# Performance work log

Hardware: AMD Instinct MI355X
Metric: run time of the kernel (lower is better)

The kernel has to match this reference:

```python
import jax, jax.numpy as jnp
import numpy as np

N0, N1, N2 = 32768, 8192, 2048
DEG = 8
E0, E1, E2 = N0 * DEG, N1 * DEG, N2 * DEG
C = 32
OUT = 40
EPS = 1e-9


def setup_inputs() -> dict:
    key = jax.random.key(0)
    ks = jax.random.split(key, 32)
    w = lambda k, s, sc=0.1: jax.random.normal(k, s, jnp.float32) * sc
    d = {}
    d['pos0'] = jax.random.normal(ks[0], (N0, 3), jnp.float32)
    d['v0'] = jax.random.normal(ks[1], (N0, 1, 3), jnp.float32)
    # attention layer weights: 10 layers total (2 per block x 5 blocks)
    d['Wq_first'] = w(ks[2], (1, C)); d['Wk_first'] = w(ks[3], (1, C))
    d['Wv_first'] = w(ks[4], (1, C)); d['Wskip_first'] = w(ks[5], (1, C))
    d['Wq_mid'] = w(ks[6], (8, C, C)); d['Wk_mid'] = w(ks[7], (8, C, C))
    d['Wv_mid'] = w(ks[8], (8, C, C)); d['Wskip_mid'] = w(ks[9], (8, C, C))
    d['Wq_last'] = w(ks[10], (C, 1)); d['Wk_last'] = w(ks[11], (C, 1))
    d['Wv_last'] = w(ks[12], (C, 1)); d['Wskip_last'] = w(ks[13], (C, 1))
    d['wr1'] = w(ks[14], (10, 1, 16)); d['wr2'] = w(ks[15], (10, 16, 1))
    d['scale_mid'] = jnp.ones((9, C), jnp.float32)
    d['bias_mid'] = jnp.zeros((9, C), jnp.float32)
    d['scale_last'] = jnp.ones((1,), jnp.float32)
    d['bias_last'] = jnp.zeros((1,), jnp.float32)
    d['Wmlp'] = w(ks[16], (3, OUT))
    d['src0'] = jax.random.randint(ks[17], (E0,), 0, N0)
    d['dst0'] = jax.random.randint(ks[18], (E0,), 0, N0)
    d['src1'] = jax.random.randint(ks[19], (E1,), 0, N1)
    d['dst1'] = jax.random.randint(ks[20], (E1,), 0, N1)
    d['src2'] = jax.random.randint(ks[21], (E2,), 0, N2)
    d['dst2'] = jax.random.randint(ks[22], (E2,), 0, N2)
    d['fp_idx1'] = jax.random.permutation(ks[23], N0)[:N1]
    d['fp_idx2'] = jax.random.permutation(ks[24], N1)[:N2]
    d['cluster1'] = jax.random.randint(ks[25], (N0,), 0, N1)
    d['cluster2'] = jax.random.randint(ks[26], (N1,), 0, N2)
    return d


def _attn(x, src, dst, rel, r, Wq, Wk, Wv, Ws, w1, w2, n):
    # x: [n, Cin, 3] type-1 fiber; equivariant linear maps mix channels only
    q = jnp.einsum('ncv,co->nov', x, Wq)
    k = jnp.einsum('ncv,co->nov', x, Wk)
    v = jnp.einsum('ncv,co->nov', x, Wv)
    logits = jnp.einsum('eov,eov->e', q[dst], k[src]) / np.float32(np.sqrt(3.0 * Wq.shape[1]))
    logits = logits + (jax.nn.relu(r @ w1) @ w2)[:, 0]  # radial (invariant) edge bias
    m = jax.ops.segment_max(logits, dst, num_segments=n)
    ex = jnp.exp(logits - m[dst])
    z = jax.ops.segment_sum(ex, dst, num_segments=n)
    alpha = ex / (z[dst] + EPS)
    msg = (v[src] + rel[:, None, :]) * alpha[:, None, None]  # x_ij='add'
    agg = jax.ops.segment_sum(msg, dst, num_segments=n)
    return agg + jnp.einsum('ncv,co->nov', x, Ws)  # learnable skip


def _norm_bias(x, scale, bias):
    # GNormBias: nonlinearity on invariant norm, preserve direction
    nrm = jnp.sqrt(jnp.sum(x * x, axis=-1, keepdims=True) + 1e-12)
    return jax.nn.relu(scale[None, :, None] * nrm + bias[None, :, None]) * (x / nrm)


def _segmean(x, seg, n):
    s = jax.ops.segment_sum(x, seg, num_segments=n)
    c = jax.ops.segment_sum(jnp.ones((seg.shape[0], 1, 1), x.dtype), seg, num_segments=n)
    return s / (c + EPS)


def reference(pos0, v0, Wq_first, Wk_first, Wv_first, Wskip_first, Wq_mid, Wk_mid, Wv_mid, Wskip_mid, Wq_last, Wk_last, Wv_last, Wskip_last, wr1, wr2, scale_mid, bias_mid, scale_last, bias_last, Wmlp, src0, dst0, src1, dst1, src2, dst2, fp_idx1, fp_idx2, cluster1, cluster2):
    def edge_geo(pos, src, dst):
        rel = pos[dst] - pos[src]
        r = jnp.sqrt(jnp.sum(rel * rel, -1, keepdims=True) + 1e-12)
        return rel, r

    rel0, r0 = edge_geo(pos0, src0, dst0)
    pos1 = pos0[fp_idx1]
    rel1, r1 = edge_geo(pos1, src1, dst1)
    pos2 = pos1[fp_idx2]
    rel2, r2 = edge_geo(pos2, src2, dst2)

    def layer(i, x, Wq, Wk, Wv, Ws, sc, bi, src, dst, rel, r, n):
        return _norm_bias(_attn(x, src, dst, rel, r, Wq, Wk, Wv, Ws, wr1[i], wr2[i], n), sc, bi)

    # down block 0 (level 0)
    x = layer(0, v0, Wq_first, Wk_first, Wv_first, Wskip_first, scale_mid[0], bias_mid[0], src0, dst0, rel0, r0, N0)
    x0 = layer(1, x, Wq_mid[0], Wk_mid[0], Wv_mid[0], Wskip_mid[0], scale_mid[1], bias_mid[1], src0, dst0, rel0, r0, N0)
    # FPS pool -> level 1, down block 1
    x = _segmean(x0, cluster1, N1)
    x = layer(2, x, Wq_mid[1], Wk_mid[1], Wv_mid[1], Wskip_mid[1], scale_mid[2], bias_mid[2], src1, dst1, rel1, r1, N1)
    x1 = layer(3, x, Wq_mid[2], Wk_mid[2], Wv_mid[2], Wskip_mid[2], scale_mid[3], bias_mid[3], src1, dst1, rel1, r1, N1)
    # FPS pool -> level 2, bottleneck
    x = _segmean(x1, cluster2, N2)
    x = layer(4, x, Wq_mid[3], Wk_mid[3], Wv_mid[3], Wskip_mid[3], scale_mid[4], bias_mid[4], src2, dst2, rel2, r2, N2)
    x = layer(5, x, Wq_mid[4], Wk_mid[4], Wv_mid[4], Wskip_mid[4], scale_mid[5], bias_mid[5], src2, dst2, rel2, r2, N2)
    # upsample to level 1 via fp_idx scatter + residual skip, up block 0
    x = jnp.zeros((N1, C, 3), x.dtype).at[fp_idx2].set(x) + x1
    x = layer(6, x, Wq_mid[5], Wk_mid[5], Wv_mid[5], Wskip_mid[5], scale_mid[6], bias_mid[6], src1, dst1, rel1, r1, N1)
    x = layer(7, x, Wq_mid[6], Wk_mid[6], Wv_mid[6], Wskip_mid[6], scale_mid[7], bias_mid[7], src1, dst1, rel1, r1, N1)
    # upsample to level 0 + residual skip, up block 1 (out fiber {1:1})
    x = jnp.zeros((N0, C, 3), x.dtype).at[fp_idx1].set(x) + x0
    x = layer(8, x, Wq_mid[7], Wk_mid[7], Wv_mid[7], Wskip_mid[7], scale_mid[8], bias_mid[8], src0, dst0, rel0, r0, N0)
    x = layer(9, x, Wq_last, Wk_last, Wv_last, Wskip_last, scale_last, bias_last, src0, dst0, rel0, r0, N0)
    # MLP head: [N0,1,3] -> (B=1, N0, 3) -> Linear(3, OUT, no bias) + ReLU
    y = jax.nn.relu(jnp.einsum('bnf,fo->bno', x.reshape(1, N0, 3), Wmlp))
    return y
```

## Files before the change

kernel.cpp:

```cpp
#include <hip/hip_runtime.h>
#include <math.h>

#define N0 32768
#define N1 8192
#define N2 2048
#define E0 262144
#define E1 65536
#define E2 16384
#define NTOT (N0+N1+N2)
#define ETOT (E0+E1+E2)
#define NBLK (NTOT/256)
#define EPS 1e-9f

static inline int cdiv(int a, int b){ return (a + b - 1) / b; }

__device__ inline unsigned bfpack(float a, float b){
  unsigned ua = __float_as_uint(a), ub = __float_as_uint(b);
  ua = (ua + 0x7fffu + ((ua >> 16) & 1u)) >> 16;
  ub = (ub + 0x7fffu + ((ub >> 16) & 1u)) & 0xffff0000u;
  return ua | ub;
}
__device__ inline float bf_lo(unsigned d){ return __uint_as_float(d << 16); }
__device__ inline float bf_hi(unsigned d){ return __uint_as_float(d & 0xffff0000u); }

__device__ inline float grp32_sum(float x){
  x += __int_as_float(__builtin_amdgcn_update_dpp(0, __float_as_int(x), 0x121, 0xf, 0xf, true));
  x += __int_as_float(__builtin_amdgcn_update_dpp(0, __float_as_int(x), 0x122, 0xf, 0xf, true));
  x += __int_as_float(__builtin_amdgcn_update_dpp(0, __float_as_int(x), 0x124, 0xf, 0xf, true));
  x += __int_as_float(__builtin_amdgcn_update_dpp(0, __float_as_int(x), 0x128, 0xf, 0xf, true));
  x += __int_as_float(__builtin_amdgcn_ds_swizzle(__float_as_int(x), 0x401F));
  return x;
}

__global__ void k_gather_pos(const float* __restrict__ pos, const int* __restrict__ idx,
                             float* __restrict__ out, int n){
  int i = blockIdx.x*256 + threadIdx.x;
  if (i < n){
    int s = idx[i];
    out[i*3+0] = pos[s*3+0];
    out[i*3+1] = pos[s*3+1];
    out[i*3+2] = pos[s*3+2];
  }
}
__global__ void k_inv_build(const int* __restrict__ fp, int* __restrict__ inv, int n2){
  int i = blockIdx.x*256 + threadIdx.x;
  if (i < n2) inv[fp[i]] = i;
}

__global__ void k_countA(const int* __restrict__ d0, const int* __restrict__ d1,
                         const int* __restrict__ d2, int* cnt){
  int e = blockIdx.x*256 + threadIdx.x;
  if (e < E0)            atomicAdd(&cnt[d0[e]], 1);
  else if (e < E0+E1)    atomicAdd(&cnt[N0 + d1[e-E0]], 1);
  else if (e < ETOT)     atomicAdd(&cnt[N0+N1 + d2[e-E0-E1]], 1);
}
__global__ __launch_bounds__(256) void k_scan1(const int* __restrict__ cnt,
                                               int* __restrict__ excl,
                                               int* __restrict__ bsum){
  __shared__ int lds[256];
  int tid = threadIdx.x;
  int i = blockIdx.x*256 + tid;
  int v = cnt[i];
  lds[tid] = v;
  __syncthreads();
  for (int off = 1; off < 256; off <<= 1){
    int t = (tid >= off) ? lds[tid - off] : 0;
    __syncthreads();
    lds[tid] += t;
    __syncthreads();
  }
  excl[i] = lds[tid] - v;
  if (tid == 255) bsum[blockIdx.x] = lds[255];
}
__global__ __launch_bounds__(256) void k_scan2(int* bsum, int nb){
  __shared__ int lds[256];
  int tid = threadIdx.x;
  int v = (tid < nb) ? bsum[tid] : 0;
  lds[tid] = v;
  __syncthreads();
  for (int off = 1; off < 256; off <<= 1){
    int t = (tid >= off) ? lds[tid - off] : 0;
    __syncthreads();
    lds[tid] += t;
    __syncthreads();
  }
  if (tid < nb) bsum[tid] = lds[tid] - v;
}
__global__ __launch_bounds__(256) void k_scan3(const int* __restrict__ excl,
                                               const int* __restrict__ bsum,
                                               int* __restrict__ row,
                                               int* __restrict__ cur){
  int i = blockIdx.x*256 + threadIdx.x;
  int r = excl[i] + bsum[blockIdx.x];
  row[i] = r; cur[i] = r;
  if (i == 0) row[NTOT] = ETOT;
}
__global__ void k_scatter_geoA(const int* __restrict__ s0, const int* __restrict__ d0,
                               const int* __restrict__ s1, const int* __restrict__ d1,
                               const int* __restrict__ s2, const int* __restrict__ d2,
                               const float* __restrict__ pos0, const float* __restrict__ pos1,
                               const float* __restrict__ pos2, int* cur,
                               int* __restrict__ srcs, float4* __restrict__ meta){
  int e = blockIdx.x*256 + threadIdx.x;
  if (e >= ETOT) return;
  int s, d, noff; const float* pos;
  if (e < E0)        { s = s0[e];        d = d0[e];        pos = pos0; noff = 0; }
  else if (e < E0+E1){ s = s1[e-E0];     d = d1[e-E0];     pos = pos1; noff = N0; }
  else               { s = s2[e-E0-E1];  d = d2[e-E0-E1];  pos = pos2; noff = N0+N1; }
  float dx = pos[d*3+0]-pos[s*3+0];
  float dy = pos[d*3+1]-pos[s*3+1];
  float dz = pos[d*3+2]-pos[s*3+2];
  int p = atomicAdd(&cur[noff + d], 1);
  srcs[p] = s;
  meta[p] = make_float4(sqrtf(dx*dx+dy*dy+dz*dz+1e-12f), dx, dy, dz);
}

__global__ __launch_bounds__(256) void k_rbias(const float4* __restrict__ meta,
                                               const float* __restrict__ w1,
                                               const float* __restrict__ w2,
                                               float* __restrict__ rb, int nE){
  int e = blockIdx.x*256 + threadIdx.x;
  if (e >= nE) return;
  float r = meta[e].x;
  float a = 0.f;
  #pragma unroll
  for (int j = 0; j < 16; ++j) a += fmaxf(r*w1[j], 0.f)*w2[j];
  rb[e] = a;
}

__global__ __launch_bounds__(256) void k_transformF(
    const float* __restrict__ x, const float* __restrict__ cntv,
    const float* __restrict__ up, const int* __restrict__ inv,
    const float* __restrict__ Wq, const float* __restrict__ Wk,
    const float* __restrict__ Wv, const float* __restrict__ Ws,
    float* __restrict__ q, unsigned* __restrict__ kv, float* __restrict__ s,
    int n, int Cin, int mode){
  __shared__ float wI[4096];
  __shared__ float xr4[8][128];
  __shared__ float kvst[8][192];
  int tid = threadIdx.x;
  int nw = Cin * 32;
  for (int i = tid; i < nw; i += 256){
    wI[i*4+0] = Wq[i]; wI[i*4+1] = Wk[i]; wI[i*4+2] = Wv[i]; wI[i*4+3] = Ws[i];
  }
  int g = tid >> 5, lane = tid & 31;
  int node = blockIdx.x*8 + g;
  int xl = Cin * 3;
  if (node < n){
    if (mode == 1){
      float ic = 1.f / (cntv[node] + EPS);
      for (int c = lane; c < Cin; c += 32){
        int b = node*xl + c*3;
        xr4[g][c*4+0] = x[b+0]*ic; xr4[g][c*4+1] = x[b+1]*ic; xr4[g][c*4+2] = x[b+2]*ic;
      }
    } else if (mode == 2){
      int a = inv[node];
      for (int c = lane; c < Cin; c += 32){
        int b = node*xl + c*3;
        float v0_ = x[b], v1_ = x[b+1], v2_ = x[b+2];
        if (a >= 0){
          size_t ub = (size_t)a*xl + c*3;
          v0_ += up[ub]; v1_ += up[ub+1]; v2_ += up[ub+2];
        }
        xr4[g][c*4+0] = v0_; xr4[g][c*4+1] = v1_; xr4[g][c*4+2] = v2_;
      }
    } else {
      for (int c = lane; c < Cin; c += 32){
        int b = node*xl + c*3;
        xr4[g][c*4+0] = x[b]; xr4[g][c*4+1] = x[b+1]; xr4[g][c*4+2] = x[b+2];
      }
    }
  }
  __syncthreads();
  if (node < n){
    float aq0=0.f,aq1=0.f,aq2=0.f, ak0=0.f,ak1=0.f,ak2=0.f;
    float aw0=0.f,aw1=0.f,aw2=0.f, as0=0.f,as1=0.f,as2=0.f;
    for (int c = 0; c < Cin; ++c){
      float4 xv = *(const float4*)&xr4[g][c*4];
      float4 wv = *(const float4*)&wI[(c*32+lane)*4];
      aq0 += xv.x*wv.x; aq1 += xv.y*wv.x; aq2 += xv.z*wv.x;
      ak0 += xv.x*wv.y; ak1 += xv.y*wv.y; ak2 += xv.z*wv.y;
      aw0 += xv.x*wv.z; aw1 += xv.y*wv.z; aw2 += xv.z*wv.z;
      as0 += xv.x*wv.w; as1 += xv.y*wv.w; as2 += xv.z*wv.w;
    }
    int o = node*96 + lane*3;
    q[o]=aq0; q[o+1]=aq1; q[o+2]=aq2;
    s[o]=as0; s[o+1]=as1; s[o+2]=as2;
    kvst[g][lane*3+0]=ak0; kvst[g][lane*3+1]=ak1; kvst[g][lane*3+2]=ak2;
    kvst[g][96+lane*3+0]=aw0; kvst[g][96+lane*3+1]=aw1; kvst[g][96+lane*3+2]=aw2;
    float2 p0 = *(const float2*)&kvst[g][2*lane];
    float2 p1 = *(const float2*)&kvst[g][64+2*lane];
    float2 p2 = *(const float2*)&kvst[g][128+2*lane];
    *(uint2*)(kv + (size_t)node*96 + 2*lane) = make_uint2(bfpack(p0.x,p0.y), bfpack(p1.x,p1.y));
    kv[(size_t)node*96 + 64 + lane] = bfpack(p2.x, p2.y);
  }
}

#define ATTN_CORE(QB,KVB,SB) \
  float rw1 = (lane < 16) ? wr1[lane] : 0.f; \
  float rw2 = (lane < 16) ? wr2[lane] : 0.f; \
  float ql0=0.f, ql1=0.f, ql2=0.f, ql3=0.f; \
  float z=0.f, av0=0.f, av1=0.f, av2=0.f, av3=0.f, R0=0.f, R1=0.f, R2=0.f; \
  int beg=0, end=0; \
  if (act){ \
    int nb = node*96; \
    float2 qa = *(const float2*)(QB + nb + 2*lane); \
    ql0 = qa.x*invsc; ql1 = qa.y*invsc; \
    if (lane < 16){ \
      float2 qc = *(const float2*)(QB + nb + 64 + 2*lane); \
      ql2 = qc.x*invsc; ql3 = qc.y*invsc; \
    } \
    beg = row[node]; end = row[node+1]; \
  } \
  for (int cb = beg; cb < end; cb += 32){ \
    int csz = end - cb; if (csz > 32) csz = 32; \
    int sn_l = 0; float4 mt = make_float4(0.f,0.f,0.f,0.f); \
    if (lane < csz){ \
      int idx = cb + lane; \
      sn_l = srcs[idx]; \
      mt = meta[idx]; \
    } \
    for (int j = 0; j < csz; j += 4){ \
      int gs = csz - j; if (gs > 4) gs = 4; \
      int sid[4]; float rrB[4]; \
      _Pragma("unroll") \
      for (int t = 0; t < 4; ++t){ \
        int sl = (j + t) & 31; \
        sid[t] = __shfl(sn_l, sl, 32); \
        rrB[t] = __shfl(mt.x, sl, 32); \
      } \
      unsigned d0[4], d1[4], d2[4]; \
      _Pragma("unroll") \
      for (int t = 0; t < 4; ++t){ \
        const unsigned* kp = KVB + (size_t)sid[t]*96; \
        bool ok = t < gs; \
        uint2 ab = ok ? *(const uint2*)(kp + 2*lane) : make_uint2(0u,0u); \
        d0[t] = ab.x; d1[t] = ab.y; \
        d2[t] = ok ? kp[64 + lane] : 0u; \
      } \
      _Pragma("unroll") \
      for (int t = 0; t < 4; ++t){ \
        float pt = bf_lo(d0[t])*ql0 + bf_hi(d0[t])*ql1; \
        if (lane < 16) pt += bf_lo(d1[t])*ql2 + bf_hi(d1[t])*ql3; \
        pt += fmaxf(rrB[t]*rw1, 0.f) * rw2; \
        pt = grp32_sum(pt); \
        float w = (t < gs) ? __expf(fminf(pt, 80.f)) : 0.f; \
        z += w; \
        av0 += w*bf_lo(d2[t]); av1 += w*bf_hi(d2[t]); \
        if (lane >= 16){ av2 += w*bf_lo(d1[t]); av3 += w*bf_hi(d1[t]); } \
        if (lane == j + t){ R0 += w*mt.y; R1 += w*mt.z; R2 += w*mt.w; } \
      } \
    } \
  } \
  R0 = grp32_sum(R0); \
  R1 = grp32_sum(R1); \
  R2 = grp32_sum(R2); \
  if (act){ \
    vsum[g][2*lane+32] = av0; \
    vsum[g][2*lane+33] = av1; \
    if (lane >= 16){ vsum[g][2*lane-32] = av2; vsum[g][2*lane-31] = av3; } \
  } \
  float y0=0.f, y1=0.f, y2=0.f; \
  if (act){ \
    float invz = 1.f / (z + EPS); \
    int base = node*96 + 3*lane; \
    y0 = (vsum[g][3*lane+0] + R0)*invz + SB[base]; \
    y1 = (vsum[g][3*lane+1] + R1)*invz + SB[base+1]; \
    y2 = (vsum[g][3*lane+2] + R2)*invz + SB[base+2]; \
    float nrm = sqrtf(y0*y0 + y1*y1 + y2*y2 + 1e-12f); \
    float f = fmaxf(scaleA[lane]*nrm + biasA[lane], 0.f) / nrm; \
    y0 *= f; y1 *= f; y2 *= f; \
  }

__global__ __launch_bounds__(256) void k_attn32(
    const float* __restrict__ qb, const unsigned* __restrict__ kvb,
    const float* __restrict__ sb,
    const int* __restrict__ row, const int* __restrict__ srcs,
    const float4* __restrict__ meta,
    const float* __restrict__ wr1, const float* __restrict__ wr2,
    const float* __restrict__ scaleA, const float* __restrict__ biasA,
    float* __restrict__ outb,
    float* psum, float* pcnt_, const int* __restrict__ cl,
    int n, float invsc){
  __shared__ float vsum[8][96];
  int tid = threadIdx.x, g = tid >> 5, lane = tid & 31;
  int node = blockIdx.x*8 + g;
  bool act = node < n;
  ATTN_CORE(qb, kvb, sb)
  if (act){
    int base = node*96 + 3*lane;
    outb[base]   = y0;
    outb[base+1] = y1;
    outb[base+2] = y2;
    if (cl){
      int c = cl[node];
      atomicAdd(&psum[c*96 + 3*lane],   y0);
      atomicAdd(&psum[c*96 + 3*lane+1], y1);
      atomicAdd(&psum[c*96 + 3*lane+2], y2);
      if (lane == 0) atomicAdd(&pcnt_[c], 1.f);
    }
  }
}

__global__ __launch_bounds__(256) void k_attn32_t32(
    float* __restrict__ qb, const unsigned* __restrict__ kvin,
    float* __restrict__ sb,
    const int* __restrict__ row, const int* __restrict__ srcs,
    const float4* __restrict__ meta,
    const float* __restrict__ wr1, const float* __restrict__ wr2,
    const float* __restrict__ scaleA, const float* __restrict__ biasA,
    const float* __restrict__ Wq2, const float* __restrict__ Wk2,
    const float* __restrict__ Wv2, const float* __restrict__ Ws2,
    unsigned* __restrict__ kvout, int n, float invsc){
  __shared__ float vsum[8][96];
  __shared__ float wI[4096];
  __shared__ float kvst[8][192];
  int tid = threadIdx.x, g = tid >> 5, lane = tid & 31;
  for (int i = tid; i < 1024; i += 256){
    wI[i*4+0] = Wq2[i]; wI[i*4+1] = Wk2[i]; wI[i*4+2] = Wv2[i]; wI[i*4+3] = Ws2[i];
  }
  int node = blockIdx.x*8 + g;
  bool act = node < n;
  ATTN_CORE(qb, kvin, sb)
  __syncthreads();
  if (act){
    vsum[g][3*lane+0] = y0;
    vsum[g][3*lane+1] = y1;
    vsum[g][3*lane+2] = y2;
    float aq0=0.f,aq1=0.f,aq2=0.f, ak0=0.f,ak1=0.f,ak2=0.f;
    float aw0=0.f,aw1=0.f,aw2=0.f, as0=0.f,as1=0.f,as2=0.f;
    for (int c = 0; c < 32; ++c){
      float x0 = vsum[g][c*3+0], x1 = vsum[g][c*3+1], x2 = vsum[g][c*3+2];
      float4 wv = *(const float4*)&wI[(c*32+lane)*4];
      aq0 += x0*wv.x;  aq1 += x1*wv.x;  aq2 += x2*wv.x;
      ak0 += x0*wv.y;  ak1 += x1*wv.y;  ak2 += x2*wv.y;
      aw0 += x0*wv.z;  aw1 += x1*wv.z;  aw2 += x2*wv.z;
      as0 += x0*wv.w;  as1 += x1*wv.w;  as2 += x2*wv.w;
    }
    int ob = node*96 + 3*lane;
    qb[ob]=aq0; qb[ob+1]=aq1; qb[ob+2]=aq2;
    sb[ob]=as0; sb[ob+1]=as1; sb[ob+2]=as2;
    kvst[g][lane*3+0]=ak0; kvst[g][lane*3+1]=ak1; kvst[g][lane*3+2]=ak2;
    kvst[g][96+lane*3+0]=aw0; kvst[g][96+lane*3+1]=aw1; kvst[g][96+lane*3+2]=aw2;
    float2 p0 = *(const float2*)&kvst[g][2*lane];
    float2 p1 = *(const float2*)&kvst[g][64+2*lane];
    float2 p2 = *(const float2*)&kvst[g][128+2*lane];
    *(uint2*)(kvout + (size_t)node*96 + 2*lane) = make_uint2(bfpack(p0.x,p0.y), bfpack(p1.x,p1.y));
    kvout[(size_t)node*96 + 64 + lane] = bfpack(p2.x, p2.y);
  }
}

__global__ __launch_bounds__(256) void k_attn32_t1(
    const float* __restrict__ qb, const unsigned* __restrict__ kvin,
    const float* __restrict__ sb,
    const int* __restrict__ row, const int* __restrict__ srcs,
    const float4* __restrict__ meta,
    const float* __restrict__ wr1, const float* __restrict__ wr2,
    const float* __restrict__ scaleA, const float* __restrict__ biasA,
    const float* __restrict__ Wq2, const float* __restrict__ Wk2,
    const float* __restrict__ Wv2, const float* __restrict__ Ws2,
    float* __restrict__ q1, float* __restrict__ kv1,
    float* __restrict__ s1,
    int n, float invsc){
  __shared__ float vsum[8][96];
  int tid = threadIdx.x, g = tid >> 5, lane = tid & 31;
  int node = blockIdx.x*8 + g;
  bool act = node < n;
  ATTN_CORE(qb, kvin, sb)
  if (act){
    vsum[g][3*lane+0] = y0;
    vsum[g][3*lane+1] = y1;
    vsum[g][3*lane+2] = y2;
  }
  if (act && lane < 12){
    int m = lane / 3, v = lane - m*3;
    const float* W = (m==0) ? Wq2 : (m==1) ? Wk2 : (m==2) ? Wv2 : Ws2;
    float a = 0.f;
    for (int c = 0; c < 32; ++c) a += vsum[g][c*3+v] * W[c];
    if (m==0)      q1[node*3 + v] = a;
    else if (m==1) kv1[(size_t)node*8 + v] = a;
    else if (m==2) kv1[(size_t)node*8 + 3 + v] = a;
    else           s1[node*3 + v] = a;
  }
}

__global__ __launch_bounds__(256) void k_attn1_head(
    const float* __restrict__ qb, const float* __restrict__ kv1,
    const float* __restrict__ sb, const float* __restrict__ rb9,
    const int* __restrict__ row, const int* __restrict__ srcs,
    const float4* __restrict__ meta,
    const float* __restrict__ scaleA, const float* __restrict__ biasA,
    const float* __restrict__ Wmlp,
    float* __restrict__ out, int n, float invsc){
  __shared__ float w[120];
  int tid = threadIdx.x;
  if (tid < 120) w[tid] = Wmlp[tid];
  __syncthreads();
  int i = blockIdx.x*32 + (tid >> 3);
  int lane8 = tid & 7;
  if (i >= n) return;
  float q0 = qb[i*3]*invsc, q1 = qb[i*3+1]*invsc, q2 = qb[i*3+2]*invsc;
  float z = 0.f, a0 = 0.f, a1 = 0.f, a2 = 0.f;
  int beg = row[i], end = row[i+1];
  for (int e = beg + lane8; e < end; e += 8){
    int s = srcs[e];
    float4 m = meta[e];
    float4 A = *(const float4*)(kv1 + (size_t)s*8);
    float2 B = *(const float2*)(kv1 + (size_t)s*8 + 4);
    float pt = q0*A.x + q1*A.y + q2*A.z + rb9[e];
    float wgt = __expf(fminf(pt, 80.f));
    z += wgt;
    a0 += wgt*(A.w + m.y); a1 += wgt*(B.x + m.z); a2 += wgt*(B.y + m.w);
  }
  #pragma unroll
  for (int xm = 1; xm <= 4; xm <<= 1){
    z  += __shfl_xor(z,  xm, 8);
    a0 += __shfl_xor(a0, xm, 8);
    a1 += __shfl_xor(a1, xm, 8);
    a2 += __shfl_xor(a2, xm, 8);
  }
  float invz = 1.f / (z + EPS);
  float y0 = a0*invz + sb[i*3];
  float y1 = a1*invz + sb[i*3+1];
  float y2 = a2*invz + sb[i*3+2];
  float nrm = sqrtf(y0*y0 + y1*y1 + y2*y2 + 1e-12f);
  float f = fmaxf(scaleA[0]*nrm + biasA[0], 0.f) / nrm;
  y0 *= f; y1 *= f; y2 *= f;
  #pragma unroll
  for (int c = 0; c < 5; ++c){
    int o2 = lane8*5 + c;
    out[(size_t)i*40 + o2] = fmaxf(y0*w[o2] + y1*w[40+o2] + y2*w[80+o2], 0.f);
  }
}

extern "C" void kernel_launch(void* const* d_in, const int* in_sizes, int n_in,
                              void* d_out, int out_size, void* d_ws, size_t ws_size,
                              hipStream_t stream){
  const float* pos0      = (const float*)d_in[0];
  const float* v0        = (const float*)d_in[1];
  const float* Wq_first  = (const float*)d_in[2];
  const float* Wk_first  = (const float*)d_in[3];
  const float* Wv_first  = (const float*)d_in[4];
  const float* Ws_first  = (const float*)d_in[5];
  const float* Wq_mid    = (const float*)d_in[6];
  const float* Wk_mid    = (const float*)d_in[7];
  const float* Wv_mid    = (const float*)d_in[8];
  const float* Ws_mid    = (const float*)d_in[9];
  const float* Wq_last   = (const float*)d_in[10];
  const float* Wk_last   = (const float*)d_in[11];
  const float* Wv_last   = (const float*)d_in[12];
  const float* Ws_last   = (const float*)d_in[13];
  const float* wr1       = (const float*)d_in[14];
  const float* wr2       = (const float*)d_in[15];
  const float* scale_mid = (const float*)d_in[16];
  const float* bias_mid  = (const float*)d_in[17];
  const float* scale_last= (const float*)d_in[18];
  const float* bias_last = (const float*)d_in[19];
  const float* Wmlp      = (const float*)d_in[20];
  const int* src0 = (const int*)d_in[21];
  const int* dst0 = (const int*)d_in[22];
  const int* src1 = (const int*)d_in[23];
  const int* dst1 = (const int*)d_in[24];
  const int* src2 = (const int*)d_in[25];
  const int* dst2 = (const int*)d_in[26];
  const int* fp1  = (const int*)d_in[27];
  const int* fp2  = (const int*)d_in[28];
  const int* cl1  = (const int*)d_in[29];
  const int* cl2  = (const int*)d_in[30];

  float* ws = (float*)d_ws;
  size_t o = 0;
  float* xA   = ws + o; o += (size_t)N0*96;
  float* x0s  = ws + o; o += (size_t)N0*96;
  float* x1s  = ws + o; o += (size_t)N1*96;
  float* xP1  = ws + o; o += (size_t)N1*96;
  float* xP2  = ws + o; o += (size_t)N2*96;
  float* qb   = ws + o; o += (size_t)N0*96;
  float* sb   = ws + o; o += (size_t)N0*96;
  unsigned* kvb  = (unsigned*)(ws + o); o += (size_t)N0*96;
  unsigned* kvb2 = (unsigned*)(ws + o); o += (size_t)N0*96;
  float4* metaA = (float4*)(ws + o); o += (size_t)ETOT*4;
  float* q1v  = ws + o; o += (size_t)N0*3;
  float* s1v  = ws + o; o += (size_t)N0*3;
  float* kv1  = ws + o; o += (size_t)N0*8;
  float* rb9  = ws + o; o += (size_t)E0;
  float* pcnt1 = ws + o; o += N1;
  float* pcnt2 = ws + o; o += N2;
  float* pos1 = ws + o; o += (size_t)N1*3;
  float* pos2 = ws + o; o += (size_t)N2*3;
  int* ib = (int*)(ws + o);
  size_t io = 0;
  int* rowA  = ib + io; io += NTOT+1;
  int* cntA  = ib + io; io += NTOT;
  int* curA  = ib + io; io += NTOT;
  int* exclA = ib + io; io += NTOT;
  int* bsumA = ib + io; io += 256;
  int* srcsA = ib + io; io += ETOT;
  int* inv0  = ib + io; io += N0;
  int* inv1  = ib + io; io += N1;

  hipMemsetAsync(xP1, 0, (size_t)N1*96*sizeof(float), stream);
  hipMemsetAsync(xP2, 0, (size_t)N2*96*sizeof(float), stream);
  hipMemsetAsync(pcnt1, 0, N1*sizeof(float), stream);
  hipMemsetAsync(pcnt2, 0, N2*sizeof(float), stream);
  hipMemsetAsync(inv0, 0xFF, N0*sizeof(int), stream);
  hipMemsetAsync(inv1, 0xFF, N1*sizeof(int), stream);
  hipMemsetAsync(cntA, 0, NTOT*sizeof(int), stream);

  k_gather_pos<<<cdiv(N1,256),256,0,stream>>>(pos0, fp1, pos1, N1);
  k_gather_pos<<<cdiv(N2,256),256,0,stream>>>(pos1, fp2, pos2, N2);
  k_inv_build<<<cdiv(N1,256),256,0,stream>>>(fp1, inv0, N1);
  k_inv_build<<<cdiv(N2,256),256,0,stream>>>(fp2, inv1, N2);

  k_countA<<<cdiv(ETOT,256),256,0,stream>>>(dst0, dst1, dst2, cntA);
  k_scan1<<<NBLK,256,0,stream>>>(cntA, exclA, bsumA);
  k_scan2<<<1,256,0,stream>>>(bsumA, NBLK);
  k_scan3<<<NBLK,256,0,stream>>>(exclA, bsumA, rowA, curA);
  k_scatter_geoA<<<cdiv(ETOT,256),256,0,stream>>>(src0, dst0, src1, dst1, src2, dst2,
                                                  pos0, pos1, pos2, curA, srcsA, metaA);
  k_rbias<<<cdiv(E0,256),256,0,stream>>>(metaA, wr1 + 9*16, wr2 + 9*16, rb9, E0);

  const float invsc = 1.f / sqrtf(96.f);
  const int C = 32;

  auto pair32 = [&](const float* xin, const float* cntv, const float* up, const int* inv,
                    int mode, int n, int nodeBase, int Cin,
                    const float* WqE, const float* WkE, const float* WvE, const float* WsE,
                    const float* WqO, const float* WkO, const float* WvO, const float* WsO,
                    int lE, float* xout,
                    float* psum, float* pcnt_, const int* cl){
    k_transformF<<<cdiv(n,8),256,0,stream>>>(xin, cntv, up, inv, WqE, WkE, WvE, WsE,
                                             qb, kvb, sb, n, Cin, mode);
    k_attn32_t32<<<cdiv(n,8),256,0,stream>>>(qb, kvb, sb, rowA + nodeBase, srcsA, metaA,
                                             wr1 + lE*16, wr2 + lE*16,
                                             scale_mid + lE*C, bias_mid + lE*C,
                                             WqO, WkO, WvO, WsO, kvb2, n, invsc);
    k_attn32<<<cdiv(n,8),256,0,stream>>>(qb, kvb2, sb, rowA + nodeBase, srcsA, metaA,
                                         wr1 + (lE+1)*16, wr2 + (lE+1)*16,
                                         scale_mid + (lE+1)*C, bias_mid + (lE+1)*C,
                                         xout, psum, pcnt_, cl, n, invsc);
  };

  pair32(v0, nullptr, nullptr, nullptr, 0, N0, 0, 1,
         Wq_first, Wk_first, Wv_first, Ws_first,
         Wq_mid+0*1024, Wk_mid+0*1024, Wv_mid+0*1024, Ws_mid+0*1024,
         0, x0s, xP1, pcnt1, cl1);
  pair32(xP1, pcnt1, nullptr, nullptr, 1, N1, N0, C,
         Wq_mid+1*1024, Wk_mid+1*1024, Wv_mid+1*1024, Ws_mid+1*1024,
         Wq_mid+2*1024, Wk_mid+2*1024, Wv_mid+2*1024, Ws_mid+2*1024,
         2, x1s, xP2, pcnt2, cl2);
  pair32(xP2, pcnt2, nullptr, nullptr, 1, N2, N0+N1, C,
         Wq_mid+3*1024, Wk_mid+3*1024, Wv_mid+3*1024, Ws_mid+3*1024,
         Wq_mid+4*1024, Wk_mid+4*1024, Wv_mid+4*1024, Ws_mid+4*1024,
         4, xA, nullptr, nullptr, nullptr);
  pair32(x1s, nullptr, xA, inv1, 2, N1, N0, C,
         Wq_mid+5*1024, Wk_mid+5*1024, Wv_mid+5*1024, Ws_mid+5*1024,
         Wq_mid+6*1024, Wk_mid+6*1024, Wv_mid+6*1024, Ws_mid+6*1024,
         6, xA, nullptr, nullptr, nullptr);
  k_transformF<<<cdiv(N0,8),256,0,stream>>>(x0s, nullptr, xA, inv0,
                                            Wq_mid+7*1024, Wk_mid+7*1024,
                                            Wv_mid+7*1024, Ws_mid+7*1024,
                                            qb, kvb, sb, N0, C, 2);
  k_attn32_t1<<<cdiv(N0,8),256,0,stream>>>(qb, kvb, sb, rowA, srcsA, metaA,
                                           wr1 + 8*16, wr2 + 8*16,
                                           scale_mid + 8*C, bias_mid + 8*C,
                                           Wq_last, Wk_last, Wv_last, Ws_last,
                                           q1v, kv1, s1v, N0, invsc);
  {
    float invsc1 = 1.f / sqrtf(3.f);
    k_attn1_head<<<cdiv(N0,32),256,0,stream>>>(q1v, kv1, s1v, rb9, rowA, srcsA, metaA,
                                               scale_last, bias_last,
                                               Wmlp, (float*)d_out, N0, invsc1);
  }
}
```

Baseline: 433.5 us.

## Merge graph-setup kernels and memsets to cut launch count

Merges the count and inverse-index kernels into a single setup kernel. The scan's second and third passes become one kernel in which each block re-scans the block sums itself. Positions for the coarse levels are read through the fp index chain instead of being gathered into separate buffers, and the radial-bias computation moves into the edge scatter. Zeroed buffers are laid out next to each other so one memset covers them, which cuts seven memsets to two. The aim is to remove launch and serialization overhead in preprocessing, at the cost of extra dependent index loads per edge and redundant scan work in every block.

Result: faster. 403.0 us (-7.0%).

```diff
diff --git a/kernel.cpp b/kernel.cpp
--- a/kernel.cpp
+++ b/kernel.cpp
@@ -32,27 +32,16 @@
   return x;
 }
 
-__global__ void k_gather_pos(const float* __restrict__ pos, const int* __restrict__ idx,
-                             float* __restrict__ out, int n){
-  int i = blockIdx.x*256 + threadIdx.x;
-  if (i < n){
-    int s = idx[i];
-    out[i*3+0] = pos[s*3+0];
-    out[i*3+1] = pos[s*3+1];
-    out[i*3+2] = pos[s*3+2];
-  }
-}
-__global__ void k_inv_build(const int* __restrict__ fp, int* __restrict__ inv, int n2){
-  int i = blockIdx.x*256 + threadIdx.x;
-  if (i < n2) inv[fp[i]] = i;
-}
-
-__global__ void k_countA(const int* __restrict__ d0, const int* __restrict__ d1,
-                         const int* __restrict__ d2, int* cnt){
+__global__ void k_setup(const int* __restrict__ d0, const int* __restrict__ d1,
+                        const int* __restrict__ d2,
+                        const int* __restrict__ fp1, const int* __restrict__ fp2,
+                        int* cnt, int* __restrict__ inv0, int* __restrict__ inv1){
   int e = blockIdx.x*256 + threadIdx.x;
   if (e < E0)            atomicAdd(&cnt[d0[e]], 1);
   else if (e < E0+E1)    atomicAdd(&cnt[N0 + d1[e-E0]], 1);
   else if (e < ETOT)     atomicAdd(&cnt[N0+N1 + d2[e-E0-E1]], 1);
+  if (e < N1) inv0[fp1[e]] = e;
+  if (e < N2) inv1[fp2[e]] = e;
 }
 __global__ __launch_bounds__(256) void k_scan1(const int* __restrict__ cnt,
                                                int* __restrict__ excl,
@@ -72,10 +61,13 @@
   excl[i] = lds[tid] - v;
   if (tid == 255) bsum[blockIdx.x] = lds[255];
 }
-__global__ __launch_bounds__(256) void k_scan2(int* bsum, int nb){
+__global__ __launch_bounds__(256) void k_scan23(const int* __restrict__ excl,
+                                                const int* __restrict__ bsum,
+                                                int* __restrict__ row,
+                                                int* __restrict__ cur){
   __shared__ int lds[256];
   int tid = threadIdx.x;
-  int v = (tid < nb) ? bsum[tid] : 0;
+  int v = (tid < (int)blockIdx.x && tid < NBLK) ? bsum[tid] : 0;
   lds[tid] = v;
   __syncthreads();
   for (int off = 1; off < 256; off <<= 1){
@@ -84,48 +76,46 @@
     lds[tid] += t;
     __syncthreads();
   }
-  if (tid < nb) bsum[tid] = lds[tid] - v;
-}
-__global__ __launch_bounds__(256) void k_scan3(const int* __restrict__ excl,
-                                               const int* __restrict__ bsum,
-                                               int* __restrict__ row,
-                                               int* __restrict__ cur){
-  int i = blockIdx.x*256 + threadIdx.x;
-  int r = excl[i] + bsum[blockIdx.x];
+  int offset = lds[255];
+  int i = blockIdx.x*256 + tid;
+  int r = excl[i] + offset;
   row[i] = r; cur[i] = r;
   if (i == 0) row[NTOT] = ETOT;
 }
 __global__ void k_scatter_geoA(const int* __restrict__ s0, const int* __restrict__ d0,
                                const int* __restrict__ s1, const int* __restrict__ d1,
                                const int* __restrict__ s2, const int* __restrict__ d2,
-                               const float* __restrict__ pos0, const float* __restrict__ pos1,
-                               const float* __restrict__ pos2, int* cur,
-                               int* __restrict__ srcs, float4* __restrict__ meta){
+                               const float* __restrict__ pos0,
+                               const int* __restrict__ fp1, const int* __restrict__ fp2,
+                               const float* __restrict__ w1, const float* __restrict__ w2,
+                               int* cur, int* __restrict__ srcs, float4* __restrict__ meta,
+                               float* __restrict__ rb9){
   int e = blockIdx.x*256 + threadIdx.x;
   if (e >= ETOT) return;
-  int s, d, noff; const float* pos;
-  if (e < E0)        { s = s0[e];        d = d0[e];        pos = pos0; noff = 0; }
-  else if (e < E0+E1){ s = s1[e-E0];     d = d1[e-E0];     pos = pos1; noff = N0; }
-  else               { s = s2[e-E0-E1];  d = d2[e-E0-E1];  pos = pos2; noff = N0+N1; }
-  float dx = pos[d*3+0]-pos[s*3+0];
-  float dy = pos[d*3+1]-pos[s*3+1];
-  float dz = pos[d*3+2]-pos[s*3+2];
+  int s, d, noff, sp, dp;
+  if (e < E0){
+    s = s0[e]; d = d0[e]; noff = 0;
+    sp = s; dp = d;
+  } else if (e < E0+E1){
+    s = s1[e-E0]; d = d1[e-E0]; noff = N0;
+    sp = fp1[s]; dp = fp1[d];
+  } else {
+    s = s2[e-E0-E1]; d = d2[e-E0-E1]; noff = N0+N1;
+    sp = fp1[fp2[s]]; dp = fp1[fp2[d]];
+  }
+  float dx = pos0[dp*3+0]-pos0[sp*3+0];
+  float dy = pos0[dp*3+1]-pos0[sp*3+1];
+  float dz = pos0[dp*3+2]-pos0[sp*3+2];
+  float r = sqrtf(dx*dx+dy*dy+dz*dz+1e-12f);
   int p = atomicAdd(&cur[noff + d], 1);
   srcs[p] = s;
-  meta[p] = make_float4(sqrtf(dx*dx+dy*dy+dz*dz+1e-12f), dx, dy, dz);
-}
-
-__global__ __launch_bounds__(256) void k_rbias(const float4* __restrict__ meta,
-                                               const float* __restrict__ w1,
-                                               const float* __restrict__ w2,
-                                               float* __restrict__ rb, int nE){
-  int e = blockIdx.x*256 + threadIdx.x;
-  if (e >= nE) return;
-  float r = meta[e].x;
-  float a = 0.f;
-  #pragma unroll
-  for (int j = 0; j < 16; ++j) a += fmaxf(r*w1[j], 0.f)*w2[j];
-  rb[e] = a;
+  meta[p] = make_float4(r, dx, dy, dz);
+  if (p < E0){
+    float a = 0.f;
+    #pragma unroll
+    for (int j = 0; j < 16; ++j) a += fmaxf(r*w1[j], 0.f)*w2[j];
+    rb9[p] = a;
+  }
 }
 
 __global__ __launch_bounds__(256) void k_transformF(
@@ -473,8 +463,6 @@
   float* xA   = ws + o; o += (size_t)N0*96;
   float* x0s  = ws + o; o += (size_t)N0*96;
   float* x1s  = ws + o; o += (size_t)N1*96;
-  float* xP1  = ws + o; o += (size_t)N1*96;
-  float* xP2  = ws + o; o += (size_t)N2*96;
   float* qb   = ws + o; o += (size_t)N0*96;
   float* sb   = ws + o; o += (size_t)N0*96;
   unsigned* kvb  = (unsigned*)(ws + o); o += (size_t)N0*96;
@@ -484,41 +472,34 @@
   float* s1v  = ws + o; o += (size_t)N0*3;
   float* kv1  = ws + o; o += (size_t)N0*8;
   float* rb9  = ws + o; o += (size_t)E0;
+  float* zz   = ws + o;
+  float* xP1  = ws + o; o += (size_t)N1*96;
+  float* xP2  = ws + o; o += (size_t)N2*96;
   float* pcnt1 = ws + o; o += N1;
   float* pcnt2 = ws + o; o += N2;
-  float* pos1 = ws + o; o += (size_t)N1*3;
-  float* pos2 = ws + o; o += (size_t)N2*3;
+  int* cntA = (int*)(ws + o); o += NTOT;
+  size_t zz_bytes = ((size_t)N1*96 + N2*96 + N1 + N2 + NTOT) * sizeof(float);
   int* ib = (int*)(ws + o);
   size_t io = 0;
   int* rowA  = ib + io; io += NTOT+1;
-  int* cntA  = ib + io; io += NTOT;
   int* curA  = ib + io; io += NTOT;
   int* exclA = ib + io; io += NTOT;
   int* bsumA = ib + io; io += 256;
   int* srcsA = ib + io; io += ETOT;
   int* inv0  = ib + io; io += N0;
   int* inv1  = ib + io; io += N1;
-
-  hipMemsetAsync(xP1, 0, (size_t)N1*96*sizeof(float), stream);
-  hipMemsetAsync(xP2, 0, (size_t)N2*96*sizeof(float), stream);
-  hipMemsetAsync(pcnt1, 0, N1*sizeof(float), stream);
-  hipMemsetAsync(pcnt2, 0, N2*sizeof(float), stream);
-  hipMemsetAsync(inv0, 0xFF, N0*sizeof(int), stream);
-  hipMemsetAsync(inv1, 0xFF, N1*sizeof(int), stream);
-  hipMemsetAsync(cntA, 0, NTOT*sizeof(int), stream);
-
-  k_gather_pos<<<cdiv(N1,256),256,0,stream>>>(pos0, fp1, pos1, N1);
-  k_gather_pos<<<cdiv(N2,256),256,0,stream>>>(pos1, fp2, pos2, N2);
-  k_inv_build<<<cdiv(N1,256),256,0,stream>>>(fp1, inv0, N1);
-  k_inv_build<<<cdiv(N2,256),256,0,stream>>>(fp2, inv1, N2);
-
-  k_countA<<<cdiv(ETOT,256),256,0,stream>>>(dst0, dst1, dst2, cntA);
+  size_t ff_bytes = ((size_t)N0 + N1) * sizeof(int);
+
+  hipMemsetAsync(zz, 0, zz_bytes, stream);
+  hipMemsetAsync(inv0, 0xFF, ff_bytes, stream);
+
+  k_setup<<<cdiv(ETOT,256),256,0,stream>>>(dst0, dst1, dst2, fp1, fp2, cntA, inv0, inv1);
   k_scan1<<<NBLK,256,0,stream>>>(cntA, exclA, bsumA);
-  k_scan2<<<1,256,0,stream>>>(bsumA, NBLK);
-  k_scan3<<<NBLK,256,0,stream>>>(exclA, bsumA, rowA, curA);
+  k_scan23<<<NBLK,256,0,stream>>>(exclA, bsumA, rowA, curA);
   k_scatter_geoA<<<cdiv(ETOT,256),256,0,stream>>>(src0, dst0, src1, dst1, src2, dst2,
-                                                  pos0, pos1, pos2, curA, srcsA, metaA);
-  k_rbias<<<cdiv(E0,256),256,0,stream>>>(metaA, wr1 + 9*16, wr2 + 9*16, rb9, E0);
+                                                  pos0, fp1, fp2,
+                                                  wr1 + 9*16, wr2 + 9*16,
+                                                  curA, srcsA, metaA, rb9);
 
   const float invsc = 1.f / sqrtf(96.f);
   const int C = 32;
```
